# Kernel optimization log

Measured on AMD Instinct MI355X. Metric: run time of the kernel, lower is better.

## Reference

```python
import jax, jax.numpy as jnp
import numpy as np

N_NODES = 100000
N_EDGES = 1600000
NUM_RELS = 8
NUM_BASES = 8
E_DIM = 32
MAX_LEN = 8
H_DIM = 64
OUT_DIM = 64


def setup_inputs() -> dict:
    key = jax.random.key(0)
    ks = jax.random.split(key, 16)
    inp = {
        'feat': jax.random.randint(ks[0], (N_NODES, MAX_LEN), 0, N_NODES, dtype=jnp.int32),
        'src': jax.random.randint(ks[1], (N_EDGES,), 0, N_NODES, dtype=jnp.int32),
        'dst': jax.random.randint(ks[2], (N_EDGES,), 0, N_NODES, dtype=jnp.int32),
        'etype': jax.random.randint(ks[3], (N_EDGES,), 0, NUM_RELS, dtype=jnp.int32),
        'norm': jax.random.uniform(ks[4], (N_EDGES, 1), dtype=jnp.float32),
        'emb_w': jax.random.normal(ks[5], (N_NODES, E_DIM), dtype=jnp.float32),
        'sm_w': jax.random.normal(ks[6], (H_DIM, E_DIM * MAX_LEN), dtype=jnp.float32) * 0.06,
        'sm_b': jax.random.normal(ks[7], (H_DIM,), dtype=jnp.float32) * 0.02,
        'V1': jax.random.normal(ks[8], (NUM_BASES, H_DIM, H_DIM), dtype=jnp.float32) * 0.12,
        'comp1': jax.random.normal(ks[9], (NUM_RELS, NUM_BASES), dtype=jnp.float32) * 0.35,
        'b1': jax.random.normal(ks[10], (H_DIM,), dtype=jnp.float32) * 0.02,
        'V2': jax.random.normal(ks[11], (NUM_BASES, H_DIM, OUT_DIM), dtype=jnp.float32) * 0.12,
        'comp2': jax.random.normal(ks[12], (NUM_RELS, NUM_BASES), dtype=jnp.float32) * 0.35,
        'b2': jax.random.normal(ks[13], (OUT_DIM,), dtype=jnp.float32) * 0.02,
    }
    return inp


def _rel_graph_conv(x, src, dst, etype, norm, V, comp, bias, num_nodes):
    # basis decomposition: W_r = sum_b comp[r,b] * V[b]  -> [R, in, out]
    W = jnp.einsum('rb,bio->rio', comp, V)
    # transform all node feats under every relation (R small) -> [R, N, out]
    H = jnp.einsum('ni,rio->rno', x, W)
    # per-edge relation-typed gather of transformed source features
    msg = H[etype, src] * norm            # [E, out]
    agg = jax.ops.segment_sum(msg, dst, num_segments=num_nodes)  # [N, out]
    return agg + bias


def reference(feat, src, dst, etype, norm, emb_w, sm_w, sm_b,
              V1, comp1, b1, V2, comp2, b2):
    n = feat.shape[0]
    # embedding lookup [N, max_len, e_dim] -> flatten -> linear size_matcher
    nf = emb_w[feat].reshape(n, -1)
    x = nf @ sm_w.T + sm_b                # [N, h_dim]
    h = _rel_graph_conv(x, src, dst, etype, norm, V1, comp1, b1, n)
    h = jax.nn.relu(h)                    # dropout p=0.0 -> identity
    out = _rel_graph_conv(h, src, dst, etype, norm, V2, comp2, b2, n)
    return out
```

## Files before the change

### kernel.cpp

```cpp
#include <hip/hip_runtime.h>

#define N_NODES 100000
#define N_PAD 100032
#define N_EDGES 1600000
#define NUM_RELS 8
#define KDIM 256
#define HD 64
#define KF 512

#define B_SHIFT 8
#define NBUCK 392
#define NBUCK_USED 391
#define NBLK_P 512
#define TPB_P 256
#define EPB 3125

typedef __attribute__((ext_vector_type(8))) short bf16x8;
typedef __attribute__((ext_vector_type(4))) float f32x4;

struct EP { int x, y; };
typedef const __attribute__((address_space(4))) EP*  ep_cptr;
typedef const __attribute__((address_space(4))) int* ci_cptr;

__device__ inline unsigned short f2bf(float f) {
    unsigned u = __float_as_uint(f);
    u += 0x7fff + ((u >> 16) & 1);
    return (unsigned short)(u >> 16);
}
__device__ inline float bf2f(unsigned short s) {
    return __uint_as_float(((unsigned)s) << 16);
}

__launch_bounds__(256)
__global__ void k_prep(const float* __restrict__ V1, const float* __restrict__ comp1,
                       const float* __restrict__ V2, const float* __restrict__ comp2,
                       const float* __restrict__ sm_w, const float* __restrict__ emb_w,
                       unsigned short* __restrict__ WpF1, unsigned short* __restrict__ WpF2,
                       unsigned short* __restrict__ smPack, unsigned* __restrict__ emb_bf) {
    int idx = blockIdx.x * 256 + threadIdx.x;
    if (idx < 65536) {
        int l = idx >> 15;
        int r = (idx >> 12) & 7;
        int k = (idx >> 6) & 63;
        int o = idx & 63;
        const float* V = l ? V2 : V1;
        const float* comp = l ? comp2 : comp1;
        float s = 0.f;
#pragma unroll
        for (int b = 0; b < 8; b++) s += comp[r * 8 + b] * V[(b * 64 + k) * 64 + o];
        int kk = r * 64 + k;
        int ss = kk >> 5, q = (kk >> 3) & 3, j = kk & 7;
        unsigned short* Wp = l ? WpF2 : WpF1;
        Wp[(((ss * 4 + q) * 64) + o) * 8 + j] = f2bf(s);
    } else if (idx < 81920) {
        int j = idx - 65536;
        int k = j >> 6, o = j & 63;
        int s = k >> 5, q = (k >> 3) & 3, jj = k & 7;
        smPack[(((s * 4 + q) * 64) + o) * 8 + jj] = f2bf(sm_w[o * KDIM + k]);
    } else {
        int j = idx - 81920;
        if (j < 1600000) {
            const float2* f2p = (const float2*)emb_w;
            float2 f = f2p[j];
            emb_bf[j] = ((unsigned)f2bf(f.x)) | (((unsigned)f2bf(f.y)) << 16);
        }
    }
}

__launch_bounds__(TPB_P)
__global__ void k_pcount(const int* __restrict__ dst, int* __restrict__ cnt) {
    __shared__ int lh[NBUCK];
    int t = threadIdx.x, blk = blockIdx.x;
    for (int b = t; b < NBUCK; b += TPB_P) lh[b] = 0;
    __syncthreads();
    int base = blk * EPB;
    for (int i = t; i < EPB; i += TPB_P) atomicAdd(&lh[dst[base + i] >> B_SHIFT], 1);
    __syncthreads();
    for (int b = t; b < NBUCK; b += TPB_P) cnt[blk * NBUCK + b] = lh[b];
}

__launch_bounds__(NBLK_P)
__global__ void k_pscan(const int* __restrict__ cnt, int* __restrict__ boffm, int* __restrict__ btot) {
    __shared__ int s[NBLK_P];
    int b = blockIdx.x, t = threadIdx.x;
    int v = cnt[t * NBUCK + b];
    s[t] = v;
    __syncthreads();
    for (int off = 1; off < NBLK_P; off <<= 1) {
        int u = (t >= off) ? s[t - off] : 0;
        __syncthreads();
        s[t] += u;
        __syncthreads();
    }
    boffm[t * NBUCK + b] = s[t] - v;
    if (t == NBLK_P - 1) btot[b] = s[NBLK_P - 1];
}

__launch_bounds__(512)
__global__ void k_bscan(const int* __restrict__ btot, int* __restrict__ bstart, int* __restrict__ rowptr8) {
    __shared__ int s[512];
    int t = threadIdx.x;
    int v = (t < NBUCK_USED) ? btot[t] : 0;
    s[t] = v;
    __syncthreads();
    for (int off = 1; off < 512; off <<= 1) {
        int u = (t >= off) ? s[t - off] : 0;
        __syncthreads();
        s[t] += u;
        __syncthreads();
    }
    bstart[t] = s[t] - v;
    if (t == 0) rowptr8[(size_t)N_NODES * 8] = N_EDGES;
}

__launch_bounds__(TPB_P)
__global__ void k_pscatter(const int* __restrict__ src, const int* __restrict__ dst,
                           const int* __restrict__ et, const float* __restrict__ norm,
                           const int* __restrict__ boffm, const int* __restrict__ bstart,
                           int2* __restrict__ staged) {
    __shared__ int ldsoff[NBUCK];
    int t = threadIdx.x, blk = blockIdx.x;
    for (int b = t; b < NBUCK; b += TPB_P) ldsoff[b] = bstart[b] + boffm[blk * NBUCK + b];
    __syncthreads();
    int base = blk * EPB;
    for (int i = t; i < EPB; i += TPB_P) {
        int e = base + i;
        int d = dst[e];
        int bu = d >> B_SHIFT;
        int pos = atomicAdd(&ldsoff[bu], 1);
        int packed = src[e] | (et[e] << 17) | ((d & 255) << 20);
        staged[pos] = make_int2(packed, __float_as_int(norm[e]));
    }
}

__launch_bounds__(512)
__global__ void k_finalize(const int2* __restrict__ staged, const int* __restrict__ bstart,
                           const int* __restrict__ btot, int* __restrict__ rowptr8,
                           int2* __restrict__ edata) {
    __shared__ int lh[2048];
    __shared__ int s512[512];
    __shared__ int lsc[2048];
    int b = blockIdx.x, t = threadIdx.x;
    int base = bstart[b];
    int cnt = btot[b];
    lh[t] = 0; lh[t + 512] = 0; lh[t + 1024] = 0; lh[t + 1536] = 0;
    __syncthreads();
    int2 held[9];
    int key[9], rank[9];
    int nh = 0;
    for (int i = t; i < cnt; i += 512) {
        int2 ed = staged[base + i];
        int k = (ed.x >> 17) & 2047;
        held[nh] = ed; key[nh] = k; rank[nh] = atomicAdd(&lh[k], 1); nh++;
    }
    __syncthreads();
    int b0 = lh[t * 4], b1 = lh[t * 4 + 1], b2 = lh[t * 4 + 2], b3 = lh[t * 4 + 3];
    int tot = b0 + b1 + b2 + b3;
    s512[t] = tot;
    __syncthreads();
    for (int off = 1; off < 512; off <<= 1) {
        int u = (t >= off) ? s512[t - off] : 0;
        __syncthreads();
        s512[t] += u;
        __syncthreads();
    }
    int excl = s512[t] - tot;
    lsc[t * 4] = excl;
    lsc[t * 4 + 1] = excl + b0;
    lsc[t * 4 + 2] = excl + b0 + b1;
    lsc[t * 4 + 3] = excl + b0 + b1 + b2;
    __syncthreads();
    int limit = (N_NODES << 3) - (b << 11);
    for (int idx = t; idx < 2048; idx += 512)
        if (idx < limit) rowptr8[(b << 11) + idx] = base + lsc[idx];
    for (int i = 0; i < nh; i++) {
        int p = base + lsc[key[i]] + rank[i];
        int srcv = held[i].x & 0x1FFFF;
        int etv  = (held[i].x >> 17) & 7;
        edata[p] = make_int2((srcv << 7) | etv, held[i].y);
    }
}

__launch_bounds__(256)
__global__ void k_sizematch(const int* __restrict__ feat, const unsigned* __restrict__ emb_bf,
                            const unsigned short* __restrict__ smPack, const float* __restrict__ sm_b,
                            unsigned short* __restrict__ xb) {
    int t = threadIdx.x;
    int wave = t >> 6, lane = t & 63;
    int q = lane >> 4, c = lane & 15;
    int n0 = blockIdx.x * 64 + wave * 16;
    int node = n0 + c;
    int nclamp = (node < N_NODES) ? node : (N_NODES - 1);
    const int4* fr = (const int4*)(feat + (size_t)nclamp * 8);
    int4 f0 = fr[0], f1 = fr[1];
    int fidx[8] = {f0.x, f0.y, f0.z, f0.w, f1.x, f1.y, f1.z, f1.w};
    f32x4 acc[4];
#pragma unroll
    for (int i = 0; i < 4; i++) acc[i] = (f32x4){0.f, 0.f, 0.f, 0.f};
    const bf16x8* B8 = (const bf16x8*)smPack;
#pragma unroll
    for (int s = 0; s < 8; s++) {
        const int4* ar = (const int4*)((const char*)emb_bf + (size_t)fidx[s] * 64);
        union { int4 i; bf16x8 v; } A;
        A.i = ar[q];
#pragma unroll
        for (int tl = 0; tl < 4; tl++) {
            bf16x8 b = B8[(s * 4 + q) * 64 + tl * 16 + c];
            acc[tl] = __builtin_amdgcn_mfma_f32_16x16x32_bf16(A.v, b, acc[tl], 0, 0, 0);
        }
    }
    int row_base = n0 + q * 4;
    bool full = (n0 + 15 < N_NODES);
#pragma unroll
    for (int tl = 0; tl < 4; tl++) {
        int o = tl * 16 + c;
        float bia = sm_b[o];
#pragma unroll
        for (int r = 0; r < 4; r++) {
            int nd = row_base + r;
            if (full || nd < N_NODES)
                xb[(size_t)nd * 64 + o] = f2bf(acc[tl][r] + bia);
        }
    }
}

__launch_bounds__(256)
__global__ void k_fused(const unsigned short* __restrict__ xin,
                        const int* __restrict__ rowptr8, const int2* __restrict__ edata,
                        const unsigned short* __restrict__ WpF, const float* __restrict__ bias,
                        float* __restrict__ outf, unsigned short* __restrict__ outb, int mode) {
    __shared__ __align__(16) unsigned short agg[16 * 520];
    int t = threadIdx.x;
    int wave = t >> 6, lane = t & 63;
    int n0 = blockIdx.x * 16;
    ep_cptr ep4 = (ep_cptr)(unsigned long long)edata;
    ci_cptr rp4 = (ci_cptr)(unsigned long long)rowptr8;
    {
        int* a4 = (int*)agg + wave * 4 * 260;
        for (int i = lane; i < 4 * 260; i += 64) a4[i] = 0;
    }
#define EF(S,k)  int x##S##k = ep4[j##S + (k)].x, y##S##k = ep4[j##S + (k)].y;
#define EFM(S,k) int q##S##k = j##S + (k); \
                 int c##S##k = (q##S##k <= last##S) ? q##S##k : last##S; \
                 c##S##k = (c##S##k < 0) ? 0 : c##S##k; \
                 int x##S##k = ep4[c##S##k].x; \
                 int y##S##k = (q##S##k <= last##S) ? ep4[c##S##k].y : 0;
#define GF(S,k)  unsigned short w##S##k = *((const unsigned short*)((const char*)xin + (x##S##k & 0x00FFFF80)) + lane);
#define CN(S,k)  { int et = x##S##k & 7; \
                   float keep = (et == prev##S) ? 1.0f : 0.0f; \
                   prev##S = et; \
                   acc##S = fmaf(__int_as_float(y##S##k), bf2f(w##S##k), acc##S * keep); \
                   unsigned bb = __float_as_uint(acc##S) + 0x8000u; \
                   aggrow##S[et * 64 + lane] = (unsigned short)(bb >> 16); }
#define EF8(S)   EF(S,0) EF(S,1) EF(S,2) EF(S,3) EF(S,4) EF(S,5) EF(S,6) EF(S,7)
#define EFM8(S)  EFM(S,0) EFM(S,1) EFM(S,2) EFM(S,3) EFM(S,4) EFM(S,5) EFM(S,6) EFM(S,7)
#define GF8(S)   GF(S,0) GF(S,1) GF(S,2) GF(S,3) GF(S,4) GF(S,5) GF(S,6) GF(S,7)
#define CN8(S)   CN(S,0) CN(S,1) CN(S,2) CN(S,3) CN(S,4) CN(S,5) CN(S,6) CN(S,7)
    for (int np = 0; np < 2; np++) {
        int lrowA = wave * 4 + np * 2;
        int lrowB = lrowA + 1;
        int nA = __builtin_amdgcn_readfirstlane(n0 + lrowA);
        int nB = nA + 1;
        int j0A = rp4[(size_t)nA * 8], j1A = rp4[(size_t)nA * 8 + 8];
        int j0B = rp4[(size_t)nB * 8], j1B = rp4[(size_t)nB * 8 + 8];
        unsigned short* aggrowA = agg + lrowA * 520;
        unsigned short* aggrowB = agg + lrowB * 520;
        float accA = 0.f, accB = 0.f;
        int prevA = -1, prevB = -1;
        int jA = j0A, jB = j0B;
        while (jA + 8 <= j1A && jB + 8 <= j1B) {
            EF8(A) EF8(B) GF8(A) GF8(B) CN8(A) CN8(B)
            jA += 8; jB += 8;
        }
        while (jA + 8 <= j1A) { EF8(A) GF8(A) CN8(A) jA += 8; }
        while (jB + 8 <= j1B) { EF8(B) GF8(B) CN8(B) jB += 8; }
        {
            int lastA = j1A - 1, lastB = j1B - 1;
            if (((j1A - jA) | (j1B - jB)) > 0) {
                EFM8(A) EFM8(B) GF8(A) GF8(B) CN8(A) CN8(B)
            }
        }
    }
#undef EF
#undef EFM
#undef GF
#undef CN
#undef EF8
#undef EFM8
#undef GF8
#undef CN8
    __syncthreads();
    int q = lane >> 4, c = lane & 15;
    int o16 = wave * 16;
    f32x4 accd = (f32x4){0.f, 0.f, 0.f, 0.f};
    const bf16x8* B8 = (const bf16x8*)WpF;
#pragma unroll
    for (int s = 0; s < 16; s++) {
        bf16x8 a = *(const bf16x8*)&agg[c * 520 + s * 32 + q * 8];
        bf16x8 bfr = B8[(s * 4 + q) * 64 + o16 + c];
        accd = __builtin_amdgcn_mfma_f32_16x16x32_bf16(a, bfr, accd, 0, 0, 0);
    }
    int col = o16 + c;
    float bia = bias[col];
#pragma unroll
    for (int r = 0; r < 4; r++) {
        int node = n0 + q * 4 + r;
        float v = accd[r] + bia;
        if (mode == 1) {
            v = fmaxf(v, 0.f);
            outb[(size_t)node * 64 + col] = f2bf(v);
        } else {
            outf[(size_t)node * 64 + col] = v;
        }
    }
}

extern "C" void kernel_launch(void* const* d_in, const int* in_sizes, int n_in,
                              void* d_out, int out_size, void* d_ws, size_t ws_size,
                              hipStream_t stream) {
    const int*   feat  = (const int*)d_in[0];
    const int*   src   = (const int*)d_in[1];
    const int*   dst   = (const int*)d_in[2];
    const int*   etype = (const int*)d_in[3];
    const float* norm  = (const float*)d_in[4];
    const float* emb_w = (const float*)d_in[5];
    const float* sm_w  = (const float*)d_in[6];
    const float* sm_b  = (const float*)d_in[7];
    const float* V1    = (const float*)d_in[8];
    const float* comp1 = (const float*)d_in[9];
    const float* b1    = (const float*)d_in[10];
    const float* V2    = (const float*)d_in[11];
    const float* comp2 = (const float*)d_in[12];
    const float* b2    = (const float*)d_in[13];
    float* out = (float*)d_out;

    char* p = (char*)d_ws;
    auto alloc = [&](size_t bytes) { void* q = (void*)p; p += (bytes + 255) & ~(size_t)255; return q; };
    unsigned short* xb     = (unsigned short*)alloc((size_t)N_PAD * 64 * 2);
    unsigned short* hb     = (unsigned short*)alloc((size_t)N_PAD * 64 * 2);
    unsigned short* WpF1   = (unsigned short*)alloc((size_t)KF * HD * 2);
    unsigned short* WpF2   = (unsigned short*)alloc((size_t)KF * HD * 2);
    unsigned short* smPack = (unsigned short*)alloc(KDIM * HD * 2);
    unsigned*       emb_bf = (unsigned*)alloc((size_t)N_NODES * 32 * 2);
    int*   cnt    = (int*)alloc((size_t)NBLK_P * NBUCK * 4);
    int*   boffm  = (int*)alloc((size_t)NBLK_P * NBUCK * 4);
    int*   btot   = (int*)alloc((size_t)NBUCK * 4);
    int*   bstart = (int*)alloc((size_t)(NBUCK + 1) * 4);
    int*   rowptr8 = (int*)alloc(((size_t)N_NODES * 8 + 1) * 4);
    int2*  staged = (int2*)alloc((size_t)N_EDGES * 8);
    int2*  edata  = (int2*)alloc((size_t)N_EDGES * 8);

    k_prep<<<6570, 256, 0, stream>>>(V1, comp1, V2, comp2, sm_w, emb_w,
                                     WpF1, WpF2, smPack, emb_bf);

    k_pcount<<<NBLK_P, TPB_P, 0, stream>>>(dst, cnt);
    k_pscan<<<NBUCK_USED, NBLK_P, 0, stream>>>(cnt, boffm, btot);
    k_bscan<<<1, 512, 0, stream>>>(btot, bstart, rowptr8);
    k_pscatter<<<NBLK_P, TPB_P, 0, stream>>>(src, dst, etype, norm, boffm, bstart, staged);
    k_finalize<<<NBUCK_USED, 512, 0, stream>>>(staged, bstart, btot, rowptr8, edata);

    k_sizematch<<<N_PAD / 64, 256, 0, stream>>>(feat, emb_bf, smPack, sm_b, xb);

    k_fused<<<N_NODES / 16, 256, 0, stream>>>(xb, rowptr8, edata, WpF1, b1, nullptr, hb, 1);
    k_fused<<<N_NODES / 16, 256, 0, stream>>>(hb, rowptr8, edata, WpF2, b2, out, nullptr, 0);
}
```

Baseline: 295.7 us.

## Merge preprocessing kernels into fewer launches and inline bucket-start scans

Folds the dst bucket counting into the weight/embedding prep kernel, merges the partitioned scatter with the size-matcher GEMM into one launch, and recomputes the bucket-start scan redundantly inside each block instead of in a separate single-block kernel. This cuts the launch count from eight to five and lets independent work share a grid, removing launch gaps and serial tiny kernels. It also sets a min-blocks hint of 8 on the fused conv kernel, which may constrain registers. The cost is redundant scan work in every scatter and finalize block.

Result: no change. 296.8 us (+0.4%).

```diff
diff --git a/kernel.cpp b/kernel.cpp
--- a/kernel.cpp
+++ b/kernel.cpp
@@ -14,6 +14,7 @@
 #define NBLK_P 512
 #define TPB_P 256
 #define EPB 3125
+#define NBLK_SM 1563
 
 typedef __attribute__((ext_vector_type(8))) short bf16x8;
 typedef __attribute__((ext_vector_type(4))) float f32x4;
@@ -32,12 +33,26 @@
 }
 
 __launch_bounds__(256)
-__global__ void k_prep(const float* __restrict__ V1, const float* __restrict__ comp1,
-                       const float* __restrict__ V2, const float* __restrict__ comp2,
-                       const float* __restrict__ sm_w, const float* __restrict__ emb_w,
-                       unsigned short* __restrict__ WpF1, unsigned short* __restrict__ WpF2,
-                       unsigned short* __restrict__ smPack, unsigned* __restrict__ emb_bf) {
-    int idx = blockIdx.x * 256 + threadIdx.x;
+__global__ void k_build1(const float* __restrict__ V1, const float* __restrict__ comp1,
+                         const float* __restrict__ V2, const float* __restrict__ comp2,
+                         const float* __restrict__ sm_w, const float* __restrict__ emb_w,
+                         const int* __restrict__ dst,
+                         unsigned short* __restrict__ WpF1, unsigned short* __restrict__ WpF2,
+                         unsigned short* __restrict__ smPack, unsigned* __restrict__ emb_bf,
+                         int* __restrict__ cnt) {
+    __shared__ int lh[NBUCK];
+    int t = threadIdx.x;
+    if (blockIdx.x < NBLK_P) {
+        int blk = blockIdx.x;
+        for (int b = t; b < NBUCK; b += TPB_P) lh[b] = 0;
+        __syncthreads();
+        int base = blk * EPB;
+        for (int i = t; i < EPB; i += TPB_P) atomicAdd(&lh[dst[base + i] >> B_SHIFT], 1);
+        __syncthreads();
+        for (int b = t; b < NBUCK; b += TPB_P) cnt[blk * NBUCK + b] = lh[b];
+        return;
+    }
+    int idx = (blockIdx.x - NBLK_P) * 256 + t;
     if (idx < 65536) {
         int l = idx >> 15;
         int r = (idx >> 12) & 7;
@@ -67,18 +82,6 @@
     }
 }
 
-__launch_bounds__(TPB_P)
-__global__ void k_pcount(const int* __restrict__ dst, int* __restrict__ cnt) {
-    __shared__ int lh[NBUCK];
-    int t = threadIdx.x, blk = blockIdx.x;
-    for (int b = t; b < NBUCK; b += TPB_P) lh[b] = 0;
-    __syncthreads();
-    int base = blk * EPB;
-    for (int i = t; i < EPB; i += TPB_P) atomicAdd(&lh[dst[base + i] >> B_SHIFT], 1);
-    __syncthreads();
-    for (int b = t; b < NBUCK; b += TPB_P) cnt[blk * NBUCK + b] = lh[b];
-}
-
 __launch_bounds__(NBLK_P)
 __global__ void k_pscan(const int* __restrict__ cnt, int* __restrict__ boffm, int* __restrict__ btot) {
     __shared__ int s[NBLK_P];
@@ -96,53 +99,116 @@
     if (t == NBLK_P - 1) btot[b] = s[NBLK_P - 1];
 }
 
+__device__ inline void bstart256(const int* __restrict__ btot, int* sB, int* bst) {
+    int t = threadIdx.x;
+    int i0 = t * 2, i1 = t * 2 + 1;
+    int v0 = (i0 < NBUCK_USED) ? btot[i0] : 0;
+    int v1 = (i1 < NBUCK_USED) ? btot[i1] : 0;
+    int pv = v0 + v1;
+    sB[t] = pv;
+    __syncthreads();
+    for (int off = 1; off < 256; off <<= 1) {
+        int u = (t >= off) ? sB[t - off] : 0;
+        __syncthreads();
+        sB[t] += u;
+        __syncthreads();
+    }
+    int excl = sB[t] - pv;
+    if (i0 < NBUCK) bst[i0] = excl;
+    if (i1 < NBUCK) bst[i1] = excl + v0;
+    __syncthreads();
+}
+
+__launch_bounds__(256)
+__global__ void k_build2(const int* __restrict__ src, const int* __restrict__ dst,
+                         const int* __restrict__ et, const float* __restrict__ norm,
+                         const int* __restrict__ boffm, const int* __restrict__ btot,
+                         int2* __restrict__ staged,
+                         const int* __restrict__ feat, const unsigned* __restrict__ emb_bf,
+                         const unsigned short* __restrict__ smPack, const float* __restrict__ sm_b,
+                         unsigned short* __restrict__ xb) {
+    __shared__ int sB[256];
+    __shared__ int bst[NBUCK];
+    __shared__ int ldsoff[NBUCK];
+    int t = threadIdx.x;
+    if (blockIdx.x < NBLK_P) {
+        int blk = blockIdx.x;
+        bstart256(btot, sB, bst);
+        for (int b = t; b < NBUCK; b += TPB_P) ldsoff[b] = bst[b] + boffm[blk * NBUCK + b];
+        __syncthreads();
+        int base = blk * EPB;
+        for (int i = t; i < EPB; i += TPB_P) {
+            int e = base + i;
+            int d = dst[e];
+            int bu = d >> B_SHIFT;
+            int pos = atomicAdd(&ldsoff[bu], 1);
+            int packed = src[e] | (et[e] << 17) | ((d & 255) << 20);
+            staged[pos] = make_int2(packed, __float_as_int(norm[e]));
+        }
+        return;
+    }
+    int wave = t >> 6, lane = t & 63;
+    int q = lane >> 4, c = lane & 15;
+    int n0 = (blockIdx.x - NBLK_P) * 64 + wave * 16;
+    int node = n0 + c;
+    int nclamp = (node < N_NODES) ? node : (N_NODES - 1);
+    const int4* fr = (const int4*)(feat + (size_t)nclamp * 8);
+    int4 f0 = fr[0], f1 = fr[1];
+    int fidx[8] = {f0.x, f0.y, f0.z, f0.w, f1.x, f1.y, f1.z, f1.w};
+    f32x4 acc[4];
+#pragma unroll
+    for (int i = 0; i < 4; i++) acc[i] = (f32x4){0.f, 0.f, 0.f, 0.f};
+    const bf16x8* B8 = (const bf16x8*)smPack;
+#pragma unroll
+    for (int s = 0; s < 8; s++) {
+        const int4* ar = (const int4*)((const char*)emb_bf + (size_t)fidx[s] * 64);
+        union { int4 i; bf16x8 v; } A;
+        A.i = ar[q];
+#pragma unroll
+        for (int tl = 0; tl < 4; tl++) {
+            bf16x8 b = B8[(s * 4 + q) * 64 + tl * 16 + c];
+            acc[tl] = __builtin_amdgcn_mfma_f32_16x16x32_bf16(A.v, b, acc[tl], 0, 0, 0);
+        }
+    }
+    int row_base = n0 + q * 4;
+    bool full = (n0 + 15 < N_NODES);
+#pragma unroll
+    for (int tl = 0; tl < 4; tl++) {
+        int o = tl * 16 + c;
+        float bia = sm_b[o];
+#pragma unroll
+        for (int r = 0; r < 4; r++) {
+            int nd = row_base + r;
+            if (full || nd < N_NODES)
+                xb[(size_t)nd * 64 + o] = f2bf(acc[tl][r] + bia);
+        }
+    }
+}
+
 __launch_bounds__(512)
-__global__ void k_bscan(const int* __restrict__ btot, int* __restrict__ bstart, int* __restrict__ rowptr8) {
-    __shared__ int s[512];
-    int t = threadIdx.x;
-    int v = (t < NBUCK_USED) ? btot[t] : 0;
-    s[t] = v;
-    __syncthreads();
-    for (int off = 1; off < 512; off <<= 1) {
-        int u = (t >= off) ? s[t - off] : 0;
-        __syncthreads();
-        s[t] += u;
-        __syncthreads();
-    }
-    bstart[t] = s[t] - v;
-    if (t == 0) rowptr8[(size_t)N_NODES * 8] = N_EDGES;
-}
-
-__launch_bounds__(TPB_P)
-__global__ void k_pscatter(const int* __restrict__ src, const int* __restrict__ dst,
-                           const int* __restrict__ et, const float* __restrict__ norm,
-                           const int* __restrict__ boffm, const int* __restrict__ bstart,
-                           int2* __restrict__ staged) {
-    __shared__ int ldsoff[NBUCK];
-    int t = threadIdx.x, blk = blockIdx.x;
-    for (int b = t; b < NBUCK; b += TPB_P) ldsoff[b] = bstart[b] + boffm[blk * NBUCK + b];
-    __syncthreads();
-    int base = blk * EPB;
-    for (int i = t; i < EPB; i += TPB_P) {
-        int e = base + i;
-        int d = dst[e];
-        int bu = d >> B_SHIFT;
-        int pos = atomicAdd(&ldsoff[bu], 1);
-        int packed = src[e] | (et[e] << 17) | ((d & 255) << 20);
-        staged[pos] = make_int2(packed, __float_as_int(norm[e]));
-    }
-}
-
-__launch_bounds__(512)
-__global__ void k_finalize(const int2* __restrict__ staged, const int* __restrict__ bstart,
-                           const int* __restrict__ btot, int* __restrict__ rowptr8,
-                           int2* __restrict__ edata) {
+__global__ void k_finalize(const int2* __restrict__ staged, const int* __restrict__ btot,
+                           int* __restrict__ rowptr8, int2* __restrict__ edata) {
     __shared__ int lh[2048];
     __shared__ int s512[512];
     __shared__ int lsc[2048];
+    __shared__ int bst[512];
     int b = blockIdx.x, t = threadIdx.x;
-    int base = bstart[b];
+    {
+        int v = (t < NBUCK_USED) ? btot[t] : 0;
+        s512[t] = v;
+        __syncthreads();
+        for (int off = 1; off < 512; off <<= 1) {
+            int u = (t >= off) ? s512[t - off] : 0;
+            __syncthreads();
+            s512[t] += u;
+            __syncthreads();
+        }
+        bst[t] = s512[t] - v;
+        __syncthreads();
+    }
+    int base = bst[b];
     int cnt = btot[b];
+    if (b == 0 && t == 0) rowptr8[(size_t)N_NODES * 8] = N_EDGES;
     lh[t] = 0; lh[t + 512] = 0; lh[t + 1024] = 0; lh[t + 1536] = 0;
     __syncthreads();
     int2 held[9];
@@ -181,50 +247,7 @@
     }
 }
 
-__launch_bounds__(256)
-__global__ void k_sizematch(const int* __restrict__ feat, const unsigned* __restrict__ emb_bf,
-                            const unsigned short* __restrict__ smPack, const float* __restrict__ sm_b,
-                            unsigned short* __restrict__ xb) {
-    int t = threadIdx.x;
-    int wave = t >> 6, lane = t & 63;
-    int q = lane >> 4, c = lane & 15;
-    int n0 = blockIdx.x * 64 + wave * 16;
-    int node = n0 + c;
-    int nclamp = (node < N_NODES) ? node : (N_NODES - 1);
-    const int4* fr = (const int4*)(feat + (size_t)nclamp * 8);
-    int4 f0 = fr[0], f1 = fr[1];
-    int fidx[8] = {f0.x, f0.y, f0.z, f0.w, f1.x, f1.y, f1.z, f1.w};
-    f32x4 acc[4];
-#pragma unroll
-    for (int i = 0; i < 4; i++) acc[i] = (f32x4){0.f, 0.f, 0.f, 0.f};
-    const bf16x8* B8 = (const bf16x8*)smPack;
-#pragma unroll
-    for (int s = 0; s < 8; s++) {
-        const int4* ar = (const int4*)((const char*)emb_bf + (size_t)fidx[s] * 64);
-        union { int4 i; bf16x8 v; } A;
-        A.i = ar[q];
-#pragma unroll
-        for (int tl = 0; tl < 4; tl++) {
-            bf16x8 b = B8[(s * 4 + q) * 64 + tl * 16 + c];
-            acc[tl] = __builtin_amdgcn_mfma_f32_16x16x32_bf16(A.v, b, acc[tl], 0, 0, 0);
-        }
-    }
-    int row_base = n0 + q * 4;
-    bool full = (n0 + 15 < N_NODES);
-#pragma unroll
-    for (int tl = 0; tl < 4; tl++) {
-        int o = tl * 16 + c;
-        float bia = sm_b[o];
-#pragma unroll
-        for (int r = 0; r < 4; r++) {
-            int nd = row_base + r;
-            if (full || nd < N_NODES)
-                xb[(size_t)nd * 64 + o] = f2bf(acc[tl][r] + bia);
-        }
-    }
-}
-
-__launch_bounds__(256)
+__launch_bounds__(256, 8)
 __global__ void k_fused(const unsigned short* __restrict__ xin,
                         const int* __restrict__ rowptr8, const int2* __restrict__ edata,
                         const unsigned short* __restrict__ WpF, const float* __restrict__ bias,
@@ -345,21 +368,16 @@
     int*   cnt    = (int*)alloc((size_t)NBLK_P * NBUCK * 4);
     int*   boffm  = (int*)alloc((size_t)NBLK_P * NBUCK * 4);
     int*   btot   = (int*)alloc((size_t)NBUCK * 4);
-    int*   bstart = (int*)alloc((size_t)(NBUCK + 1) * 4);
     int*   rowptr8 = (int*)alloc(((size_t)N_NODES * 8 + 1) * 4);
     int2*  staged = (int2*)alloc((size_t)N_EDGES * 8);
     int2*  edata  = (int2*)alloc((size_t)N_EDGES * 8);
 
-    k_prep<<<6570, 256, 0, stream>>>(V1, comp1, V2, comp2, sm_w, emb_w,
-                                     WpF1, WpF2, smPack, emb_bf);
-
-    k_pcount<<<NBLK_P, TPB_P, 0, stream>>>(dst, cnt);
+    k_build1<<<NBLK_P + 6570, 256, 0, stream>>>(V1, comp1, V2, comp2, sm_w, emb_w, dst,
+                                                WpF1, WpF2, smPack, emb_bf, cnt);
     k_pscan<<<NBUCK_USED, NBLK_P, 0, stream>>>(cnt, boffm, btot);
-    k_bscan<<<1, 512, 0, stream>>>(btot, bstart, rowptr8);
-    k_pscatter<<<NBLK_P, TPB_P, 0, stream>>>(src, dst, etype, norm, boffm, bstart, staged);
-    k_finalize<<<NBUCK_USED, 512, 0, stream>>>(staged, bstart, btot, rowptr8, edata);
-
-    k_sizematch<<<N_PAD / 64, 256, 0, stream>>>(feat, emb_bf, smPack, sm_b, xb);
+    k_build2<<<NBLK_P + NBLK_SM, 256, 0, stream>>>(src, dst, etype, norm, boffm, btot, staged,
+                                                   feat, emb_bf, smPack, sm_b, xb);
+    k_finalize<<<NBUCK_USED, 512, 0, stream>>>(staged, btot, rowptr8, edata);
 
     k_fused<<<N_NODES / 16, 256, 0, stream>>>(xb, rowptr8, edata, WpF1, b1, nullptr, hb, 1);
     k_fused<<<N_NODES / 16, 256, 0, stream>>>(hb, rowptr8, edata, WpF2, b2, out, nullptr, 0);
```
